# Kernel tuning notes

Hardware: AMD Instinct MI355X
Metric: run time of the kernel (lower is better)

The kernel has to match this reference:

```python
import jax, jax.numpy as jnp
import numpy as np

N, R, H, OUT = 512, 16, 16, 1
EPSILON = 1e-6
CUTOFF = 5.0  # ExpNormalSmearing cutoff_upper (cutoff_lower = 0)


def exp_normal_smearing(dist):
    # dist: (N, N, 1) -> (N, N, R); TorchMD-Net style ExpNormalSmearing
    start = jnp.exp(-CUTOFF)
    means = jnp.linspace(start, 1.0, R, dtype=dist.dtype)
    beta = (2.0 / R * (1.0 - start)) ** -2
    cutoff = 0.5 * (jnp.cos(dist * jnp.pi / CUTOFF) + 1.0) * (dist < CUTOFF)
    return cutoff * jnp.exp(-beta * (jnp.exp(-dist) - means) ** 2)


def setup_inputs() -> dict:
    key = jax.random.key(0)
    ks = jax.random.split(key, 9)
    s_in = 1.0 / np.sqrt(H * H)
    s_h = 1.0 / np.sqrt(H)
    return {
        "x": jax.random.normal(ks[0], (N, 3), jnp.float32) * 1.5,
        "W": jax.random.normal(ks[1], (2, N, R, H), jnp.float32) * 0.1,
        "W1": jax.random.normal(ks[2], (H, H * H), jnp.float32) * s_in,
        "b1": jax.random.normal(ks[3], (H,), jnp.float32) * 0.01,
        "W2": jax.random.normal(ks[4], (4 * R * H, H), jnp.float32) * s_h,
        "W3": jax.random.normal(ks[5], (H, H * H), jnp.float32) * s_in,
        "b3": jax.random.normal(ks[6], (H,), jnp.float32) * 0.01,
        "W4": jax.random.normal(ks[7], (OUT, H), jnp.float32) * s_h,
        "b4": jax.random.normal(ks[8], (OUT,), jnp.float32) * 0.01,
    }


def reference(x, W, W1, b1, W2, W3, b3, W4, b4):
    K, Q = W[0], W[1]                               # (N, R, H) each
    diff = x[:, None, :] - x[None, :, :]            # (N, N, 3)
    nsq = jnp.sum(diff * diff, axis=-1, keepdims=True) + EPSILON
    norm = jnp.sqrt(nsq)                            # (N, N, 1)
    diff = diff / nsq                               # note: divided by squared norm (faithful)
    sm = exp_normal_smearing(norm)                  # (N, N, R)
    basis = sm[..., None] * diff[..., None, :]      # (N, N, R, 3)

    bk = jnp.einsum('ijrb,jrc->icb', basis, K)      # (N, H, 3)
    bq = jnp.einsum('ijrb,jrc->icb', basis, Q)
    att = jnp.einsum('ihb,igb->ihg', bk, bq).reshape(N, H * H)
    att = jax.nn.silu(att @ W1.T + b1) @ W2.T       # (N, 4*R*H), second Linear bias-free

    left, right = att[:, : 2 * R * H], att[:, 2 * R * H:]
    pair = left[:, None, :] + right[None, :, :]     # (N, N, 2*R*H)
    K2 = pair[..., : R * H].reshape(N, N, R, H)
    Q2 = pair[..., R * H:].reshape(N, N, R, H)

    bk = jnp.einsum('ijrb,ijrc->icb', basis, K2)    # (N, H, 3)
    bq = jnp.einsum('ijrb,ijrc->icb', basis, Q2)
    att = jnp.einsum('ihb,igb->ihg', bk, bq).reshape(N, H * H)
    return jax.nn.silu(att @ W3.T + b3) @ W4.T + b4  # (N, OUT)
```

## Files before the change

### kernel.cpp

```cpp
#include <hip/hip_runtime.h>
#include <hip/hip_bf16.h>
#include <math.h>

#define NN 512

#define START 0.006737946999085467f
#define STEP  ((1.0f - START) * (1.0f/15.0f))
#define SB    (0.125f * (1.0f - START))
#define BETA  (1.0f/(SB*SB))
#define LOG2E 1.4426950408889634f
#define NB    (-(BETA)*LOG2E)


__global__ __launch_bounds__(256) void k1a(const float* __restrict__ x,
                                           const float* __restrict__ W,
                                           float* __restrict__ part1)
{
    const int ib = blockIdx.x >> 1, jsH = blockIdx.x & 1;
    const int i0 = ib * 4;
    const int tid = threadIdx.x;
    const int c = tid & 15, js = tid >> 4;
    const int lane = tid & 63, wv = tid >> 6;

    __shared__ float lK[16*272];
    __shared__ float lQ[16*272];
    __shared__ float lG[4*272];
    __shared__ float lD[192];
    __shared__ float s_part[4][16][26];

    const int gi = tid >> 6, gj = (tid >> 2) & 15, grq = tid & 3;
    const float gxi0 = x[(i0+gi)*3+0];
    const float gxi1 = x[(i0+gi)*3+1];
    const float gxi2 = x[(i0+gi)*3+2];

    float acc[24];
    #pragma unroll
    for (int v = 0; v < 24; ++v) acc[v] = 0.f;

    for (int jt = 0; jt < 16; ++jt) {
        const int jb = jsH*256 + jt*16;
        __syncthreads();

        #pragma unroll
        for (int k = 0; k < 8; ++k) {
            int idx = tid + k*256;
            int arr = idx >> 10, rem = idx & 1023;
            int j = rem >> 6, q = rem & 63;
            int r = q >> 2, cq = q & 3;
            float4 v4 = *reinterpret_cast<const float4*>(
                W + arr*NN*256 + (jb+j)*256 + r*16 + cq*4);
            float* dst = (arr ? lQ : lK) + j*272 + r*17 + cq*4;
            dst[0]=v4.x; dst[1]=v4.y; dst[2]=v4.z; dst[3]=v4.w;
        }

        {
            float d0 = gxi0 - x[(jb+gj)*3+0];
            float d1 = gxi1 - x[(jb+gj)*3+1];
            float d2 = gxi2 - x[(jb+gj)*3+2];
            float nsq = fmaf(d0,d0, fmaf(d1,d1, fmaf(d2,d2, 1e-6f)));
            float rs  = __builtin_amdgcn_rsqf(nsq);
            float nrm = nsq * rs;
            float inv = rs * rs;
            float cutv = 0.f;
            if (nrm < 5.0f) cutv = 0.5f*(__cosf(nrm*0.6283185307179586f)+1.0f);
            float en = exp2f(-LOG2E * nrm);
            if (grq == 0) {
                lD[(gi*16+gj)*3+0] = d0*inv;
                lD[(gi*16+gj)*3+1] = d1*inv;
                lD[(gi*16+gj)*3+2] = d2*inv;
            }
            #pragma unroll
            for (int k = 0; k < 4; ++k) {
                int r = grq*4 + k;
                float t = en - (START + STEP*(float)r);
                lG[gi*272 + gj*17 + r] = cutv * exp2f(NB*t*t);
            }
        }
        __syncthreads();

        float kk[16], qq[16];
        #pragma unroll
        for (int r = 0; r < 16; ++r) {
            kk[r] = lK[js*272 + r*17 + c];
            qq[r] = lQ[js*272 + r*17 + c];
        }
        #pragma unroll
        for (int i = 0; i < 4; ++i) {
            float tk = 0.f, tq = 0.f;
            #pragma unroll
            for (int r = 0; r < 16; ++r) {
                float g = lG[i*272 + js*17 + r];
                tk = fmaf(g, kk[r], tk);
                tq = fmaf(g, qq[r], tq);
            }
            float dd0 = lD[(i*16+js)*3+0];
            float dd1 = lD[(i*16+js)*3+1];
            float dd2 = lD[(i*16+js)*3+2];
            acc[i*6+0] = fmaf(tk, dd0, acc[i*6+0]);
            acc[i*6+1] = fmaf(tk, dd1, acc[i*6+1]);
            acc[i*6+2] = fmaf(tk, dd2, acc[i*6+2]);
            acc[i*6+3] = fmaf(tq, dd0, acc[i*6+3]);
            acc[i*6+4] = fmaf(tq, dd1, acc[i*6+4]);
            acc[i*6+5] = fmaf(tq, dd2, acc[i*6+5]);
        }
    }

    #pragma unroll
    for (int v = 0; v < 24; ++v) {
        float t = acc[v];
        t += __shfl_xor(t, 16);
        t += __shfl_xor(t, 32);
        if (lane < 16) s_part[wv][c][v] = t;
    }
    __syncthreads();

    for (int v = tid; v < 384; v += 256) {
        int i = v / 96, o = v - i*96;
        int kq = o / 48, rem = o - kq*48;
        int b = rem >> 4, c2 = rem & 15;
        int f = i*6 + kq*3 + b;
        float sum = s_part[0][c2][f] + s_part[1][c2][f]
                  + s_part[2][c2][f] + s_part[3][c2][f];
        part1[(i0+i)*192 + jsH*96 + o] = sum;
    }
}

__global__ __launch_bounds__(256) void k1b(const float* __restrict__ part1,
                                           const float* __restrict__ W1,
                                           const float* __restrict__ b1,
                                           const float* __restrict__ W2,
                                           float* __restrict__ att2)
{
    const int i = blockIdx.x;
    const int tid = threadIdx.x;
    __shared__ float s_bkq[96];
    __shared__ float s_att[256];
    __shared__ float s_z[16][16];
    __shared__ float s_a1[16];

    if (tid < 96) {
        const float* p = part1 + i*192 + tid;
        s_bkq[tid] = p[0] + p[96];
    }
    __syncthreads();

    {
        int h = tid >> 4, g = tid & 15;
        s_att[tid] = s_bkq[     h]*s_bkq[48+     g]
                   + s_bkq[16 + h]*s_bkq[48+16 + g]
                   + s_bkq[32 + h]*s_bkq[48+32 + g];
    }
    __syncthreads();

    {
        int h = tid & 15, seg = tid >> 4;
        const float* w1 = W1 + h*256 + seg*16;
        const float* a  = s_att + seg*16;
        float p = 0.f;
        #pragma unroll
        for (int k = 0; k < 16; ++k) p = fmaf(a[k], w1[k], p);
        s_z[seg][h] = p;
    }
    __syncthreads();

    if (tid < 16) {
        float z = b1[tid];
        #pragma unroll
        for (int seg = 0; seg < 16; ++seg) z += s_z[seg][tid];
        s_a1[tid] = z / (1.0f + __expf(-z));
    }
    __syncthreads();

    float a1[16];
    #pragma unroll
    for (int c = 0; c < 16; ++c) a1[c] = s_a1[c];
    #pragma unroll
    for (int p = 0; p < 4; ++p) {
        int o = tid + p*256;
        const float4* w2 = reinterpret_cast<const float4*>(W2 + o*16);
        float4 wa = w2[0], wb = w2[1], wc = w2[2], wd = w2[3];
        float accv = wa.x*a1[0] + wa.y*a1[1] + wa.z*a1[2] + wa.w*a1[3]
                   + wb.x*a1[4] + wb.y*a1[5] + wb.z*a1[6] + wb.w*a1[7]
                   + wc.x*a1[8] + wc.y*a1[9] + wc.z*a1[10]+ wc.w*a1[11]
                   + wd.x*a1[12]+ wd.y*a1[13]+ wd.z*a1[14]+ wd.w*a1[15];
        att2[i*1024 + o] = accv;
    }
}

__global__ __launch_bounds__(256) void k2a(const float* __restrict__ x,
                                           const float* __restrict__ att2,
                                           float* __restrict__ part2)
{
    const int ib = blockIdx.x >> 1, jsH = blockIdx.x & 1;
    const int i0 = ib * 4;
    const int tid = threadIdx.x;
    const int c = tid & 15, js = tid >> 4;
    const int lane = tid & 63, wv = tid >> 6;

    __shared__ float lK[16*272];
    __shared__ float lQ[16*272];
    __shared__ float lG[4*272];
    __shared__ float lD[192];
    __shared__ float s_part[4][16][38];

    const int gi = tid >> 6, gj = (tid >> 2) & 15, grq = tid & 3;
    const float gxi0 = x[(i0+gi)*3+0];
    const float gxi1 = x[(i0+gi)*3+1];
    const float gxi2 = x[(i0+gi)*3+2];

    float acc[36];
    #pragma unroll
    for (int v = 0; v < 36; ++v) acc[v] = 0.f;

    for (int jt = 0; jt < 16; ++jt) {
        const int jb = jsH*256 + jt*16;
        __syncthreads();

        #pragma unroll
        for (int k = 0; k < 8; ++k) {
            int idx = tid + k*256;
            int arr = idx >> 10, rem = idx & 1023;
            int j = rem >> 6, q = rem & 63;
            int r = q >> 2, cq = q & 3;
            float4 v4 = *reinterpret_cast<const float4*>(
                att2 + (jb+j)*1024 + 512 + arr*256 + r*16 + cq*4);
            float* dst = (arr ? lQ : lK) + j*272 + r*17 + cq*4;
            dst[0]=v4.x; dst[1]=v4.y; dst[2]=v4.z; dst[3]=v4.w;
        }

        {
            float d0 = gxi0 - x[(jb+gj)*3+0];
            float d1 = gxi1 - x[(jb+gj)*3+1];
            float d2 = gxi2 - x[(jb+gj)*3+2];
            float nsq = fmaf(d0,d0, fmaf(d1,d1, fmaf(d2,d2, 1e-6f)));
            float rs  = __builtin_amdgcn_rsqf(nsq);
            float nrm = nsq * rs;
            float inv = rs * rs;
            float cutv = 0.f;
            if (nrm < 5.0f) cutv = 0.5f*(__cosf(nrm*0.6283185307179586f)+1.0f);
            float en = exp2f(-LOG2E * nrm);
            if (grq == 0) {
                lD[(gi*16+gj)*3+0] = d0*inv;
                lD[(gi*16+gj)*3+1] = d1*inv;
                lD[(gi*16+gj)*3+2] = d2*inv;
            }
            #pragma unroll
            for (int k = 0; k < 4; ++k) {
                int r = grq*4 + k;
                float t = en - (START + STEP*(float)r);
                lG[gi*272 + gj*17 + r] = cutv * exp2f(NB*t*t);
            }
        }
        __syncthreads();

        float kk[16], qq[16];
        #pragma unroll
        for (int r = 0; r < 16; ++r) {
            kk[r] = lK[js*272 + r*17 + c];
            qq[r] = lQ[js*272 + r*17 + c];
        }
        #pragma unroll
        for (int i = 0; i < 4; ++i) {
            float tk = 0.f, tq = 0.f;
            #pragma unroll
            for (int r = 0; r < 16; ++r) {
                float g = lG[i*272 + js*17 + r];
                tk = fmaf(g, kk[r], tk);
                tq = fmaf(g, qq[r], tq);
            }
            float dd0 = lD[(i*16+js)*3+0];
            float dd1 = lD[(i*16+js)*3+1];
            float dd2 = lD[(i*16+js)*3+2];
            acc[i*6+0] = fmaf(tk, dd0, acc[i*6+0]);
            acc[i*6+1] = fmaf(tk, dd1, acc[i*6+1]);
            acc[i*6+2] = fmaf(tk, dd2, acc[i*6+2]);
            acc[i*6+3] = fmaf(tq, dd0, acc[i*6+3]);
            acc[i*6+4] = fmaf(tq, dd1, acc[i*6+4]);
            acc[i*6+5] = fmaf(tq, dd2, acc[i*6+5]);
            float gc = lG[i*272 + js*17 + c];
            acc[24+i*3+0] = fmaf(gc, dd0, acc[24+i*3+0]);
            acc[24+i*3+1] = fmaf(gc, dd1, acc[24+i*3+1]);
            acc[24+i*3+2] = fmaf(gc, dd2, acc[24+i*3+2]);
        }
    }

    #pragma unroll
    for (int v = 0; v < 36; ++v) {
        float t = acc[v];
        t += __shfl_xor(t, 16);
        t += __shfl_xor(t, 32);
        if (lane < 16) s_part[wv][c][v] = t;
    }
    __syncthreads();

    for (int v = tid; v < 576; v += 256) {
        int i = v / 144, o = v - i*144;
        int c2, f;
        if (o < 96) {
            int kq = o / 48, rem = o - kq*48;
            int b = rem >> 4; c2 = rem & 15;
            f = i*6 + kq*3 + b;
        } else {
            int oS = o - 96;
            int r = oS / 3, b = oS - r*3;
            c2 = r;
            f = 24 + i*3 + b;
        }
        float sum = s_part[0][c2][f] + s_part[1][c2][f]
                  + s_part[2][c2][f] + s_part[3][c2][f];
        part2[(i0+i)*288 + jsH*144 + o] = sum;
    }
}

__global__ __launch_bounds__(256) void k2b(const float* __restrict__ att2,
                                           const float* __restrict__ part2,
                                           const float* __restrict__ W3,
                                           const float* __restrict__ b3,
                                           const float* __restrict__ W4,
                                           const float* __restrict__ b4,
                                           float* __restrict__ out)
{
    const int i = blockIdx.x;
    const int tid = threadIdx.x;
    __shared__ float s_red[144];
    __shared__ float s_att[256];
    __shared__ float s_z[16][16];
    __shared__ float s_a1[16];

    if (tid < 144) {
        const float* p = part2 + i*288 + tid;
        s_red[tid] = p[0] + p[144];
    }
    __syncthreads();

    if (tid < 96) {
        int kq = tid / 48, rem = tid - kq*48;
        int b = rem >> 4, c = rem & 15;
        const float* lrow = att2 + i*1024 + kq*256 + c;
        float add = 0.f;
        #pragma unroll
        for (int r = 0; r < 16; ++r)
            add = fmaf(lrow[r*16], s_red[96 + r*3 + b], add);
        s_red[tid] += add;
    }
    __syncthreads();

    {
        int h = tid >> 4, g = tid & 15;
        s_att[tid] = s_red[     h]*s_red[48+     g]
                   + s_red[16 + h]*s_red[48+16 + g]
                   + s_red[32 + h]*s_red[48+32 + g];
    }
    __syncthreads();

    {
        int h = tid & 15, seg = tid >> 4;
        const float* w3 = W3 + h*256 + seg*16;
        const float* a  = s_att + seg*16;
        float p = 0.f;
        #pragma unroll
        for (int k = 0; k < 16; ++k) p = fmaf(a[k], w3[k], p);
        s_z[seg][h] = p;
    }
    __syncthreads();

    if (tid < 16) {
        float z = b3[tid];
        #pragma unroll
        for (int seg = 0; seg < 16; ++seg) z += s_z[seg][tid];
        s_a1[tid] = z / (1.0f + __expf(-z));
    }
    __syncthreads();

    if (tid == 0) {
        float accv = b4[0];
        #pragma unroll
        for (int c = 0; c < 16; ++c) accv = fmaf(s_a1[c], W4[c], accv);
        out[i] = accv;
    }
}

extern "C" void kernel_launch(void* const* d_in, const int* in_sizes, int n_in,
                              void* d_out, int out_size, void* d_ws, size_t ws_size,
                              hipStream_t stream) {
    (void)in_sizes; (void)n_in; (void)out_size; (void)ws_size;
    const float* x  = (const float*)d_in[0];
    const float* W  = (const float*)d_in[1];
    const float* W1 = (const float*)d_in[2];
    const float* b1 = (const float*)d_in[3];
    const float* W2 = (const float*)d_in[4];
    const float* W3 = (const float*)d_in[5];
    const float* b3 = (const float*)d_in[6];
    const float* W4 = (const float*)d_in[7];
    const float* b4 = (const float*)d_in[8];

    float* att2  = (float*)d_ws;
    float* part1 = att2 + 512*1024;
    float* part2 = part1 + 512*192;
    float* out   = (float*)d_out;

    k1a<<<256, 256, 0, stream>>>(x, W, part1);
    k1b<<<512, 256, 0, stream>>>(part1, W1, b1, W2, att2);
    k2a<<<256, 256, 0, stream>>>(x, att2, part2);
    k2b<<<512, 256, 0, stream>>>(att2, part2, W3, b3, W4, b4, out);
}
```

Measured before the change: 143.3 us.

## Split j-range eightfold, read K/Q directly from global, vectorize LDS layout

The two pair-sum kernels now split the j dimension into 8 chunks instead of 2, launching 1024 blocks rather than 256, so more work runs in parallel across the CUs. The consumer kernels now reduce 8 partials instead of 2. The shared-memory staging of the K/Q tiles is removed, and each thread reads its 16 strided values straight from global memory, relying on cache. The smearing and direction buffers are re-laid out as padded float4 rows for vector LDS access. The costs are more partial-sum traffic and uncoalesced strided global loads.

```diff
diff --git a/kernel.cpp b/kernel.cpp
--- a/kernel.cpp
+++ b/kernel.cpp
@@ -16,16 +16,14 @@
                                            const float* __restrict__ W,
                                            float* __restrict__ part1)
 {
-    const int ib = blockIdx.x >> 1, jsH = blockIdx.x & 1;
+    const int ib = blockIdx.x & 127, jsH = blockIdx.x >> 7;
     const int i0 = ib * 4;
     const int tid = threadIdx.x;
     const int c = tid & 15, js = tid >> 4;
     const int lane = tid & 63, wv = tid >> 6;
 
-    __shared__ float lK[16*272];
-    __shared__ float lQ[16*272];
-    __shared__ float lG[4*272];
-    __shared__ float lD[192];
+    __shared__ float lG[1328];
+    __shared__ float lP[256];
     __shared__ float s_part[4][16][26];
 
     const int gi = tid >> 6, gj = (tid >> 2) & 15, grq = tid & 3;
@@ -37,21 +35,9 @@
     #pragma unroll
     for (int v = 0; v < 24; ++v) acc[v] = 0.f;
 
-    for (int jt = 0; jt < 16; ++jt) {
-        const int jb = jsH*256 + jt*16;
+    for (int jt = 0; jt < 4; ++jt) {
+        const int jb = jsH*64 + jt*16;
         __syncthreads();
-
-        #pragma unroll
-        for (int k = 0; k < 8; ++k) {
-            int idx = tid + k*256;
-            int arr = idx >> 10, rem = idx & 1023;
-            int j = rem >> 6, q = rem & 63;
-            int r = q >> 2, cq = q & 3;
-            float4 v4 = *reinterpret_cast<const float4*>(
-                W + arr*NN*256 + (jb+j)*256 + r*16 + cq*4);
-            float* dst = (arr ? lQ : lK) + j*272 + r*17 + cq*4;
-            dst[0]=v4.x; dst[1]=v4.y; dst[2]=v4.z; dst[3]=v4.w;
-        }
 
         {
             float d0 = gxi0 - x[(jb+gj)*3+0];
@@ -65,43 +51,58 @@
             if (nrm < 5.0f) cutv = 0.5f*(__cosf(nrm*0.6283185307179586f)+1.0f);
             float en = exp2f(-LOG2E * nrm);
             if (grq == 0) {
-                lD[(gi*16+gj)*3+0] = d0*inv;
-                lD[(gi*16+gj)*3+1] = d1*inv;
-                lD[(gi*16+gj)*3+2] = d2*inv;
+                float4 dP; dP.x = d0*inv; dP.y = d1*inv; dP.z = d2*inv; dP.w = 0.f;
+                *reinterpret_cast<float4*>(&lP[(gi*16+gj)*4]) = dP;
             }
-            #pragma unroll
-            for (int k = 0; k < 4; ++k) {
-                int r = grq*4 + k;
-                float t = en - (START + STEP*(float)r);
-                lG[gi*272 + gj*17 + r] = cutv * exp2f(NB*t*t);
+            float4 g4;
+            {
+                float t0 = en - (START + STEP*(float)(grq*4+0));
+                float t1 = en - (START + STEP*(float)(grq*4+1));
+                float t2 = en - (START + STEP*(float)(grq*4+2));
+                float t3 = en - (START + STEP*(float)(grq*4+3));
+                g4.x = cutv * exp2f(NB*t0*t0);
+                g4.y = cutv * exp2f(NB*t1*t1);
+                g4.z = cutv * exp2f(NB*t2*t2);
+                g4.w = cutv * exp2f(NB*t3*t3);
             }
+            *reinterpret_cast<float4*>(&lG[gi*328 + gj*20 + grq*4]) = g4;
         }
         __syncthreads();
 
+        const float* Kr = W + (size_t)(jb+js)*256 + c;
+        const float* Qr = Kr + NN*256;
         float kk[16], qq[16];
         #pragma unroll
-        for (int r = 0; r < 16; ++r) {
-            kk[r] = lK[js*272 + r*17 + c];
-            qq[r] = lQ[js*272 + r*17 + c];
-        }
+        for (int r = 0; r < 16; ++r) { kk[r] = Kr[r*16]; qq[r] = Qr[r*16]; }
+
         #pragma unroll
         for (int i = 0; i < 4; ++i) {
+            const float4* gp = reinterpret_cast<const float4*>(&lG[i*328 + js*20]);
+            float4 gA = gp[0], gB = gp[1], gC = gp[2], gD = gp[3];
             float tk = 0.f, tq = 0.f;
-            #pragma unroll
-            for (int r = 0; r < 16; ++r) {
-                float g = lG[i*272 + js*17 + r];
-                tk = fmaf(g, kk[r], tk);
-                tq = fmaf(g, qq[r], tq);
-            }
-            float dd0 = lD[(i*16+js)*3+0];
-            float dd1 = lD[(i*16+js)*3+1];
-            float dd2 = lD[(i*16+js)*3+2];
-            acc[i*6+0] = fmaf(tk, dd0, acc[i*6+0]);
-            acc[i*6+1] = fmaf(tk, dd1, acc[i*6+1]);
-            acc[i*6+2] = fmaf(tk, dd2, acc[i*6+2]);
-            acc[i*6+3] = fmaf(tq, dd0, acc[i*6+3]);
-            acc[i*6+4] = fmaf(tq, dd1, acc[i*6+4]);
-            acc[i*6+5] = fmaf(tq, dd2, acc[i*6+5]);
+            tk = fmaf(gA.x,kk[ 0], tk); tq = fmaf(gA.x,qq[ 0], tq);
+            tk = fmaf(gA.y,kk[ 1], tk); tq = fmaf(gA.y,qq[ 1], tq);
+            tk = fmaf(gA.z,kk[ 2], tk); tq = fmaf(gA.z,qq[ 2], tq);
+            tk = fmaf(gA.w,kk[ 3], tk); tq = fmaf(gA.w,qq[ 3], tq);
+            tk = fmaf(gB.x,kk[ 4], tk); tq = fmaf(gB.x,qq[ 4], tq);
+            tk = fmaf(gB.y,kk[ 5], tk); tq = fmaf(gB.y,qq[ 5], tq);
+            tk = fmaf(gB.z,kk[ 6], tk); tq = fmaf(gB.z,qq[ 6], tq);
+            tk = fmaf(gB.w,kk[ 7], tk); tq = fmaf(gB.w,qq[ 7], tq);
+            tk = fmaf(gC.x,kk[ 8], tk); tq = fmaf(gC.x,qq[ 8], tq);
+            tk = fmaf(gC.y,kk[ 9], tk); tq = fmaf(gC.y,qq[ 9], tq);
+            tk = fmaf(gC.z,kk[10], tk); tq = fmaf(gC.z,qq[10], tq);
+            tk = fmaf(gC.w,kk[11], tk); tq = fmaf(gC.w,qq[11], tq);
+            tk = fmaf(gD.x,kk[12], tk); tq = fmaf(gD.x,qq[12], tq);
+            tk = fmaf(gD.y,kk[13], tk); tq = fmaf(gD.y,qq[13], tq);
+            tk = fmaf(gD.z,kk[14], tk); tq = fmaf(gD.z,qq[14], tq);
+            tk = fmaf(gD.w,kk[15], tk); tq = fmaf(gD.w,qq[15], tq);
+            float4 dd = *reinterpret_cast<const float4*>(&lP[(i*16+js)*4]);
+            acc[i*6+0] = fmaf(tk, dd.x, acc[i*6+0]);
+            acc[i*6+1] = fmaf(tk, dd.y, acc[i*6+1]);
+            acc[i*6+2] = fmaf(tk, dd.z, acc[i*6+2]);
+            acc[i*6+3] = fmaf(tq, dd.x, acc[i*6+3]);
+            acc[i*6+4] = fmaf(tq, dd.y, acc[i*6+4]);
+            acc[i*6+5] = fmaf(tq, dd.z, acc[i*6+5]);
         }
     }
 
@@ -121,7 +122,7 @@
         int f = i*6 + kq*3 + b;
         float sum = s_part[0][c2][f] + s_part[1][c2][f]
                   + s_part[2][c2][f] + s_part[3][c2][f];
-        part1[(i0+i)*192 + jsH*96 + o] = sum;
+        part1[(i0+i)*768 + jsH*96 + o] = sum;
     }
 }
 
@@ -139,8 +140,11 @@
     __shared__ float s_a1[16];
 
     if (tid < 96) {
-        const float* p = part1 + i*192 + tid;
-        s_bkq[tid] = p[0] + p[96];
+        const float* p = part1 + i*768 + tid;
+        float s = 0.f;
+        #pragma unroll
+        for (int k = 0; k < 8; ++k) s += p[k*96];
+        s_bkq[tid] = s;
     }
     __syncthreads();
 
@@ -173,7 +177,7 @@
 
     float a1[16];
     #pragma unroll
-    for (int c = 0; c < 16; ++c) a1[c] = s_a1[c];
+    for (int cc = 0; cc < 16; ++cc) a1[cc] = s_a1[cc];
     #pragma unroll
     for (int p = 0; p < 4; ++p) {
         int o = tid + p*256;
@@ -191,16 +195,14 @@
                                            const float* __restrict__ att2,
                                            float* __restrict__ part2)
 {
-    const int ib = blockIdx.x >> 1, jsH = blockIdx.x & 1;
+    const int ib = blockIdx.x & 127, jsH = blockIdx.x >> 7;
     const int i0 = ib * 4;
     const int tid = threadIdx.x;
     const int c = tid & 15, js = tid >> 4;
     const int lane = tid & 63, wv = tid >> 6;
 
-    __shared__ float lK[16*272];
-    __shared__ float lQ[16*272];
-    __shared__ float lG[4*272];
-    __shared__ float lD[192];
+    __shared__ float lG[1328];
+    __shared__ float lP[256];
     __shared__ float s_part[4][16][38];
 
     const int gi = tid >> 6, gj = (tid >> 2) & 15, grq = tid & 3;
@@ -212,21 +214,9 @@
     #pragma unroll
     for (int v = 0; v < 36; ++v) acc[v] = 0.f;
 
-    for (int jt = 0; jt < 16; ++jt) {
-        const int jb = jsH*256 + jt*16;
+    for (int jt = 0; jt < 4; ++jt) {
+        const int jb = jsH*64 + jt*16;
         __syncthreads();
-
-        #pragma unroll
-        for (int k = 0; k < 8; ++k) {
-            int idx = tid + k*256;
-            int arr = idx >> 10, rem = idx & 1023;
-            int j = rem >> 6, q = rem & 63;
-            int r = q >> 2, cq = q & 3;
-            float4 v4 = *reinterpret_cast<const float4*>(
-                att2 + (jb+j)*1024 + 512 + arr*256 + r*16 + cq*4);
-            float* dst = (arr ? lQ : lK) + j*272 + r*17 + cq*4;
-            dst[0]=v4.x; dst[1]=v4.y; dst[2]=v4.z; dst[3]=v4.w;
-        }
 
         {
             float d0 = gxi0 - x[(jb+gj)*3+0];
@@ -240,47 +230,62 @@
             if (nrm < 5.0f) cutv = 0.5f*(__cosf(nrm*0.6283185307179586f)+1.0f);
             float en = exp2f(-LOG2E * nrm);
             if (grq == 0) {
-                lD[(gi*16+gj)*3+0] = d0*inv;
-                lD[(gi*16+gj)*3+1] = d1*inv;
-                lD[(gi*16+gj)*3+2] = d2*inv;
+                float4 dP; dP.x = d0*inv; dP.y = d1*inv; dP.z = d2*inv; dP.w = 0.f;
+                *reinterpret_cast<float4*>(&lP[(gi*16+gj)*4]) = dP;
             }
-            #pragma unroll
-            for (int k = 0; k < 4; ++k) {
-                int r = grq*4 + k;
-                float t = en - (START + STEP*(float)r);
-                lG[gi*272 + gj*17 + r] = cutv * exp2f(NB*t*t);
+            float4 g4;
+            {
+                float t0 = en - (START + STEP*(float)(grq*4+0));
+                float t1 = en - (START + STEP*(float)(grq*4+1));
+                float t2 = en - (START + STEP*(float)(grq*4+2));
+                float t3 = en - (START + STEP*(float)(grq*4+3));
+                g4.x = cutv * exp2f(NB*t0*t0);
+                g4.y = cutv * exp2f(NB*t1*t1);
+                g4.z = cutv * exp2f(NB*t2*t2);
+                g4.w = cutv * exp2f(NB*t3*t3);
             }
+            *reinterpret_cast<float4*>(&lG[gi*328 + gj*20 + grq*4]) = g4;
         }
         __syncthreads();
 
+        const float* Rk = att2 + (size_t)(jb+js)*1024 + 512 + c;
+        const float* Rq = Rk + 256;
         float kk[16], qq[16];
         #pragma unroll
-        for (int r = 0; r < 16; ++r) {
-            kk[r] = lK[js*272 + r*17 + c];
-            qq[r] = lQ[js*272 + r*17 + c];
-        }
+        for (int r = 0; r < 16; ++r) { kk[r] = Rk[r*16]; qq[r] = Rq[r*16]; }
+
         #pragma unroll
         for (int i = 0; i < 4; ++i) {
+            const float4* gp = reinterpret_cast<const float4*>(&lG[i*328 + js*20]);
+            float4 gA = gp[0], gB = gp[1], gC = gp[2], gD = gp[3];
             float tk = 0.f, tq = 0.f;
-            #pragma unroll
-            for (int r = 0; r < 16; ++r) {
-                float g = lG[i*272 + js*17 + r];
-                tk = fmaf(g, kk[r], tk);
-                tq = fmaf(g, qq[r], tq);
-            }
-            float dd0 = lD[(i*16+js)*3+0];
-            float dd1 = lD[(i*16+js)*3+1];
-            float dd2 = lD[(i*16+js)*3+2];
-            acc[i*6+0] = fmaf(tk, dd0, acc[i*6+0]);
-            acc[i*6+1] = fmaf(tk, dd1, acc[i*6+1]);
-            acc[i*6+2] = fmaf(tk, dd2, acc[i*6+2]);
-            acc[i*6+3] = fmaf(tq, dd0, acc[i*6+3]);
-            acc[i*6+4] = fmaf(tq, dd1, acc[i*6+4]);
-            acc[i*6+5] = fmaf(tq, dd2, acc[i*6+5]);
-            float gc = lG[i*272 + js*17 + c];
-            acc[24+i*3+0] = fmaf(gc, dd0, acc[24+i*3+0]);
-            acc[24+i*3+1] = fmaf(gc, dd1, acc[24+i*3+1]);
-            acc[24+i*3+2] = fmaf(gc, dd2, acc[24+i*3+2]);
+            tk = fmaf(gA.x,kk[ 0], tk); tq = fmaf(gA.x,qq[ 0], tq);
+            tk = fmaf(gA.y,kk[ 1], tk); tq = fmaf(gA.y,qq[ 1], tq);
+            tk = fmaf(gA.z,kk[ 2], tk); tq = fmaf(gA.z,qq[ 2], tq);
+            tk = fmaf(gA.w,kk[ 3], tk); tq = fmaf(gA.w,qq[ 3], tq);
+            tk = fmaf(gB.x,kk[ 4], tk); tq = fmaf(gB.x,qq[ 4], tq);
+            tk = fmaf(gB.y,kk[ 5], tk); tq = fmaf(gB.y,qq[ 5], tq);
+            tk = fmaf(gB.z,kk[ 6], tk); tq = fmaf(gB.z,qq[ 6], tq);
+            tk = fmaf(gB.w,kk[ 7], tk); tq = fmaf(gB.w,qq[ 7], tq);
+            tk = fmaf(gC.x,kk[ 8], tk); tq = fmaf(gC.x,qq[ 8], tq);
+            tk = fmaf(gC.y,kk[ 9], tk); tq = fmaf(gC.y,qq[ 9], tq);
+            tk = fmaf(gC.z,kk[10], tk); tq = fmaf(gC.z,qq[10], tq);
+            tk = fmaf(gC.w,kk[11], tk); tq = fmaf(gC.w,qq[11], tq);
+            tk = fmaf(gD.x,kk[12], tk); tq = fmaf(gD.x,qq[12], tq);
+            tk = fmaf(gD.y,kk[13], tk); tq = fmaf(gD.y,qq[13], tq);
+            tk = fmaf(gD.z,kk[14], tk); tq = fmaf(gD.z,qq[14], tq);
+            tk = fmaf(gD.w,kk[15], tk); tq = fmaf(gD.w,qq[15], tq);
+            float4 dd = *reinterpret_cast<const float4*>(&lP[(i*16+js)*4]);
+            acc[i*6+0] = fmaf(tk, dd.x, acc[i*6+0]);
+            acc[i*6+1] = fmaf(tk, dd.y, acc[i*6+1]);
+            acc[i*6+2] = fmaf(tk, dd.z, acc[i*6+2]);
+            acc[i*6+3] = fmaf(tq, dd.x, acc[i*6+3]);
+            acc[i*6+4] = fmaf(tq, dd.y, acc[i*6+4]);
+            acc[i*6+5] = fmaf(tq, dd.z, acc[i*6+5]);
+            float gc = lG[i*328 + js*20 + c];
+            acc[24+i*3+0] = fmaf(gc, dd.x, acc[24+i*3+0]);
+            acc[24+i*3+1] = fmaf(gc, dd.y, acc[24+i*3+1]);
+            acc[24+i*3+2] = fmaf(gc, dd.z, acc[24+i*3+2]);
         }
     }
 
@@ -308,7 +313,7 @@
         }
         float sum = s_part[0][c2][f] + s_part[1][c2][f]
                   + s_part[2][c2][f] + s_part[3][c2][f];
-        part2[(i0+i)*288 + jsH*144 + o] = sum;
+        part2[(i0+i)*1152 + jsH*144 + o] = sum;
     }
 }
 
@@ -328,8 +333,11 @@
     __shared__ float s_a1[16];
 
     if (tid < 144) {
-        const float* p = part2 + i*288 + tid;
-        s_red[tid] = p[0] + p[144];
+        const float* p = part2 + i*1152 + tid;
+        float s = 0.f;
+        #pragma unroll
+        for (int k = 0; k < 8; ++k) s += p[k*144];
+        s_red[tid] = s;
     }
     __syncthreads();
 
@@ -375,7 +383,7 @@
     if (tid == 0) {
         float accv = b4[0];
         #pragma unroll
-        for (int c = 0; c < 16; ++c) accv = fmaf(s_a1[c], W4[c], accv);
+        for (int cc = 0; cc < 16; ++cc) accv = fmaf(s_a1[cc], W4[cc], accv);
         out[i] = accv;
     }
 }
@@ -396,11 +404,11 @@
 
     float* att2  = (float*)d_ws;
     float* part1 = att2 + 512*1024;
-    float* part2 = part1 + 512*192;
+    float* part2 = part1 + 512*768;
     float* out   = (float*)d_out;
 
-    k1a<<<256, 256, 0, stream>>>(x, W, part1);
+    k1a<<<1024, 256, 0, stream>>>(x, W, part1);
     k1b<<<512, 256, 0, stream>>>(part1, W1, b1, W2, att2);
-    k2a<<<256, 256, 0, stream>>>(x, att2, part2);
+    k2a<<<1024, 256, 0, stream>>>(x, att2, part2);
     k2b<<<512, 256, 0, stream>>>(att2, part2, W3, b3, W4, b4, out);
 }
```

Measured after the change: 126.0 us. -12.0%, faster.
